# Performance work log

Hardware: AMD Instinct MI355X
Metric: run time of the kernel (lower is better)

The kernel has to match this reference:

```python
import jax, jax.numpy as jnp
import numpy as np

NUM_EMBEDDINGS = 4096
EMBEDDING_DIM = 512
N_TOKENS = 32768
COMMITMENT_COST = 0.25


def setup_inputs() -> dict:
    key = jax.random.key(0)
    k1, k2 = jax.random.split(key)
    flat_input = jax.random.normal(k1, (N_TOKENS, EMBEDDING_DIM), dtype=jnp.float32)
    # torch init: uniform(-1/K, 1/K)
    weight = jax.random.uniform(k2, (NUM_EMBEDDINGS, EMBEDDING_DIM), dtype=jnp.float32,
                                minval=-1.0 / NUM_EMBEDDINGS, maxval=1.0 / NUM_EMBEDDINGS)
    return {"flat_input": flat_input, "weight": weight}


def reference(flat_input, weight):
    distances = (jnp.sum(flat_input ** 2, axis=1, keepdims=True)
                 + jnp.sum(weight ** 2, axis=1)
                 - 2.0 * jnp.matmul(flat_input, weight.T))
    encoding_indices = jnp.argmin(distances, axis=1)  # [N]
    # one-hot @ weight == direct gather of codebook rows
    quantized = weight[encoding_indices]  # [N, D]

    e_latent_loss = jnp.mean((jax.lax.stop_gradient(quantized) - flat_input) ** 2, axis=1)
    q_latent_loss = jnp.mean((quantized - jax.lax.stop_gradient(flat_input)) ** 2, axis=1)
    loss = q_latent_loss + COMMITMENT_COST * e_latent_loss  # [N]

    # straight-through estimator
    quantized_st = flat_input + jax.lax.stop_gradient(quantized - flat_input)

    # avg_probs = mean of one-hot encodings over batch = normalized code counts
    counts = jnp.zeros((NUM_EMBEDDINGS,), dtype=flat_input.dtype).at[encoding_indices].add(1.0)
    avg_probs = counts / flat_input.shape[0]
    perplexity = jnp.exp(-jnp.sum(avg_probs * jnp.log(avg_probs + 1e-10)))

    return quantized_st, loss, perplexity, encoding_indices
```

## Files before the change

### kernel.cpp

```cpp
#include <hip/hip_runtime.h>
#include <math.h>

#define N_TOK 32768
#define K_CODES 4096
#define DIM 512
#define COMMIT 0.25f
#define NCAND 8
#define NSPLIT 2
#define SPLIT_CODES (K_CODES / NSPLIT)
#define NITER (SPLIT_CODES / 256)
#define BIAS 0.125f

typedef short s16x8 __attribute__((ext_vector_type(8)));
typedef float f32x4 __attribute__((ext_vector_type(4)));
typedef unsigned int uint32;
typedef unsigned long long u64;
typedef unsigned short u16;

__device__ __forceinline__ u16 f2bf(float f) {
    uint32 b = __float_as_uint(f);
    return (u16)((b + 0x7FFFu + ((b >> 16) & 1u)) >> 16);
}

__device__ __forceinline__ void gload16(const u16* g, u16* l) {
    __builtin_amdgcn_global_load_lds(
        (const __attribute__((address_space(1))) void*)g,
        (__attribute__((address_space(3))) void*)l,
        16, 0, 0);
}

__global__ __launch_bounds__(256) void tobf16_kernel(const float* __restrict__ src,
                                                     u16* __restrict__ dst, int n4) {
    int i = blockIdx.x * 256 + threadIdx.x;
    int stride = gridDim.x * 256;
    for (; i < n4; i += stride) {
        float4 v = ((const float4*)src)[i];
        ushort4 o;
        o.x = f2bf(v.x); o.y = f2bf(v.y); o.z = f2bf(v.z); o.w = f2bf(v.w);
        ((ushort4*)dst)[i] = o;
    }
}

__global__ __launch_bounds__(256) void rowsq_np_kernel(const float* __restrict__ a,
                                                       float* __restrict__ out,
                                                       int nrows) {
    #pragma clang fp contract(off)
    const int gw   = (blockIdx.x * 256 + threadIdx.x) >> 6;
    const int lane = threadIdx.x & 63;
    const int row  = gw * 8 + (lane >> 3);
    const int j    = lane & 7;
    if (row >= nrows) return;
    const float* p = a + (size_t)row * DIM;
    float blk[4];
    #pragma unroll
    for (int b = 0; b < 4; ++b) {
        const float* q = p + b * 128;
        float v = q[j];
        float r = v * v;
        for (int i = 8; i < 128; i += 8) { float u = q[i + j]; r += u * u; }
        float s1 = r  + __shfl_xor(r, 1);
        float s2 = s1 + __shfl_xor(s1, 2);
        float s3 = s2 + __shfl_xor(s2, 4);
        blk[b] = s3;
    }
    float res = (blk[0] + blk[1]) + (blk[2] + blk[3]);
    if (j == 0) out[row] = res;
}

__global__ __launch_bounds__(512, 1) void screen_kernel(const u16* __restrict__ xb,
                                                        const u16* __restrict__ wb,
                                                        const float* __restrict__ w2f,
                                                        u64* __restrict__ candPart) {
    __shared__ __attribute__((aligned(16))) u16 POOL[77824];

    const int tid  = threadIdx.x;
    const int wv   = tid >> 6;
    const int wt   = wv >> 2;
    const int wc   = wv & 3;
    const int lane = tid & 63;
    const int quad = lane >> 4;
    const int n15  = lane & 15;
    const int m0   = blockIdx.x * 128;
    const int sbase = blockIdx.y * SPLIT_CODES;

    const int l8  = lane >> 3;
    const int qsw = (lane & 7) ^ l8;

    const u16* xg0 = xb + (size_t)(m0 + wv * 16 + l8) * DIM + qsw * 8;
    const u16* xg1 = xg0 + (size_t)8 * DIM;
    const u16* wg0 = wb + (size_t)(sbase + wv * 32 + 0  + l8) * DIM + qsw * 8;
    const u16* wg1 = wg0 + (size_t)8 * DIM;
    const u16* wg2 = wg0 + (size_t)16 * DIM;
    const u16* wg3 = wg0 + (size_t)24 * DIM;

    {
        float* w2l = (float*)&POOL[73728];
        for (int i = tid; i < SPLIT_CODES; i += 512)
            w2l[i] = w2f[sbase + i] + BIAS;
    }

    uint32 r1[16], r2[16];
    #pragma unroll
    for (int i = 0; i < 16; ++i) { r1[i] = 0xFFFFFFFFu; r2[i] = 0xFFFFFFFFu; }

    f32x4 acc[4][4];
    #pragma unroll
    for (int i = 0; i < 4; ++i)
        #pragma unroll
        for (int c = 0; c < 4; ++c) acc[i][c] = (f32x4){0.f, 0.f, 0.f, 0.f};

    int xoff0[4], woff0[4], xoff1[4], woff1[4];
    #pragma unroll
    for (int i = 0; i < 4; ++i) {
        const int tr = wt * 64 + i * 16 + n15;
        xoff0[i] = tr * 64 + ((quad)     ^ (tr & 7)) * 8;
        xoff1[i] = tr * 64 + ((4 + quad) ^ (tr & 7)) * 8;
    }
    #pragma unroll
    for (int c = 0; c < 4; ++c) {
        const int cr = wc * 64 + c * 16 + n15;
        woff0[c] = cr * 64 + ((quad)     ^ (cr & 7)) * 8;
        woff1[c] = cr * 64 + ((4 + quad) ^ (cr & 7)) * 8;
    }

    #pragma unroll
    for (int tt = 0; tt < 2; ++tt) {
        const int ko = tt * 64;
        gload16(xg0 + ko, &POOL[tt * 8192 + wv * 1024]);
        gload16(xg1 + ko, &POOL[tt * 8192 + wv * 1024 + 512]);
        gload16(wg0 + ko, &POOL[24576 + tt * 16384 + wv * 2048]);
        gload16(wg1 + ko, &POOL[24576 + tt * 16384 + wv * 2048 + 512]);
        gload16(wg2 + ko, &POOL[24576 + tt * 16384 + wv * 2048 + 1024]);
        gload16(wg3 + ko, &POOL[24576 + tt * 16384 + wv * 2048 + 1536]);
    }
    __syncthreads();

    s16x8 pa[4], pb[4];
    #pragma unroll
    for (int i = 0; i < 4; ++i) pa[i] = *(const s16x8*)&POOL[xoff0[i]];
    #pragma unroll
    for (int c = 0; c < 4; ++c) pb[c] = *(const s16x8*)&POOL[24576 + woff0[c]];

    int bufc = 0;
    for (int t = 0; t < 64; ++t) {
        __syncthreads();

        if (t <= 61) {
            const int bn  = (bufc == 0) ? 2 : bufc - 1;
            const int tn  = t + 2;
            const size_t co = (size_t)(tn >> 3) * (256 * DIM) + (tn & 7) * 64;
            const size_t xo = (size_t)((tn & 7) * 64);
            gload16(xg0 + xo, &POOL[bn * 8192 + wv * 1024]);
            gload16(xg1 + xo, &POOL[bn * 8192 + wv * 1024 + 512]);
            gload16(wg0 + co, &POOL[24576 + bn * 16384 + wv * 2048]);
            gload16(wg1 + co, &POOL[24576 + bn * 16384 + wv * 2048 + 512]);
            gload16(wg2 + co, &POOL[24576 + bn * 16384 + wv * 2048 + 1024]);
            gload16(wg3 + co, &POOL[24576 + bn * 16384 + wv * 2048 + 1536]);
        }

        const u16* X = &POOL[bufc * 8192];
        const u16* W = &POOL[24576 + bufc * 16384];

        s16x8 qa[4], qb[4];
        #pragma unroll
        for (int i = 0; i < 4; ++i) qa[i] = *(const s16x8*)&X[xoff1[i]];
        #pragma unroll
        for (int c = 0; c < 4; ++c) qb[c] = *(const s16x8*)&W[woff1[c]];

        #pragma unroll
        for (int i = 0; i < 4; ++i)
            #pragma unroll
            for (int c = 0; c < 4; ++c)
                acc[i][c] = __builtin_amdgcn_mfma_f32_16x16x32_bf16(pa[i], pb[c], acc[i][c], 0, 0, 0);

        if (t < 63) {
            const int bn1 = (bufc == 2) ? 0 : bufc + 1;
            const u16* Xn = &POOL[bn1 * 8192];
            const u16* Wn = &POOL[24576 + bn1 * 16384];
            #pragma unroll
            for (int i = 0; i < 4; ++i) pa[i] = *(const s16x8*)&Xn[xoff0[i]];
            #pragma unroll
            for (int c = 0; c < 4; ++c) pb[c] = *(const s16x8*)&Wn[woff0[c]];
        }

        #pragma unroll
        for (int i = 0; i < 4; ++i)
            #pragma unroll
            for (int c = 0; c < 4; ++c)
                acc[i][c] = __builtin_amdgcn_mfma_f32_16x16x32_bf16(qa[i], qb[c], acc[i][c], 0, 0, 0);

        if ((t & 7) == 7) {
            const int it = t >> 3;
            const float* w2l = (const float*)&POOL[73728];
            float w2pb[4];
            #pragma unroll
            for (int c = 0; c < 4; ++c)
                w2pb[c] = w2l[it * 256 + wc * 64 + c * 16 + n15];
            #pragma unroll
            for (int i = 0; i < 4; ++i)
                #pragma unroll
                for (int r = 0; r < 4; ++r) {
                    const int ti = i * 4 + r;
                    #pragma unroll
                    for (int c = 0; c < 4; ++c) {
                        float s = fmaf(-2.0f, acc[i][c][r], w2pb[c]);
                        uint32 key = (__float_as_uint(s) & 0xFFFFFFC0u) | (uint32)((it << 2) | c);
                        uint32 mx = r1[ti] > key ? r1[ti] : key;
                        r1[ti] = r1[ti] < key ? r1[ti] : key;
                        r2[ti] = r2[ti] < mx ? r2[ti] : mx;
                    }
                }
            #pragma unroll
            for (int i = 0; i < 4; ++i)
                #pragma unroll
                for (int c = 0; c < 4; ++c) acc[i][c] = (f32x4){0.f, 0.f, 0.f, 0.f};
        }

        bufc = (bufc == 2) ? 0 : bufc + 1;
    }

    u64* MS = (u64*)POOL;
    for (int phase = 0; phase < 2; ++phase) {
        __syncthreads();
        if (wt == phase) {
            #pragma unroll
            for (int ti = 0; ti < 16; ++ti) {
                const int i = ti >> 2, r = ti & 3;
                const int tloc = i * 16 + quad * 4 + r;
                #pragma unroll
                for (int e = 0; e < 2; ++e) {
                    uint32 k  = e ? r2[ti] : r1[ti];
                    uint32 vb = k & 0xFFFFFFC0u;
                    uint32 id = k & 63u;
                    uint32 code = (uint32)(sbase + (id >> 2) * 256 + wc * 64 + (id & 3) * 16 + n15);
                    MS[tloc * 128 + (wc * 16 + n15) * 2 + e] = ((u64)vb << 32) | code;
                }
            }
        }
        __syncthreads();
        if (tid < 64) {
            u64 best[6];
            #pragma unroll
            for (int c = 0; c < 6; ++c) best[c] = 0xFFFFFFFFFFFFFFFFull;
            for (int e = 0; e < 128; ++e) {
                u64 v = MS[tid * 128 + e];
                if (v < best[5]) {
                    best[5] = v;
                    #pragma unroll
                    for (int p = 5; p > 0; --p)
                        if (best[p] < best[p - 1]) { u64 tv = best[p]; best[p] = best[p - 1]; best[p - 1] = tv; }
                }
            }
            const int token = m0 + phase * 64 + tid;
            u64* dst = candPart + ((size_t)blockIdx.y * N_TOK + token) * 6;
            #pragma unroll
            for (int c = 0; c < 6; ++c) dst[c] = best[c];
        }
    }
}

__global__ __launch_bounds__(256) void mergecand_kernel(const u64* __restrict__ candPart,
                                                        int* __restrict__ candF) {
    int t = blockIdx.x * 256 + threadIdx.x;
    u64 best[NCAND];
    #pragma unroll
    for (int c = 0; c < NCAND; ++c) best[c] = 0xFFFFFFFFFFFFFFFFull;
    for (int s = 0; s < NSPLIT; ++s) {
        const u64* src = candPart + ((size_t)s * N_TOK + t) * 6;
        #pragma unroll
        for (int c = 0; c < 6; ++c) {
            u64 v = src[c];
            if (v < best[NCAND - 1]) {
                best[NCAND - 1] = v;
                #pragma unroll
                for (int p = NCAND - 1; p > 0; --p)
                    if (best[p] < best[p - 1]) { u64 tv = best[p]; best[p] = best[p - 1]; best[p - 1] = tv; }
            }
        }
    }
    #pragma unroll
    for (int c = 0; c < NCAND; ++c) candF[(size_t)t * NCAND + c] = (int)(best[c] & 0xFFFu);
}

__global__ __launch_bounds__(256) void refine_kernel(const float* __restrict__ x,
                                                     const float* __restrict__ w,
                                                     const float* __restrict__ x2np,
                                                     const float* __restrict__ w2np,
                                                     const int* __restrict__ cand,
                                                     int* __restrict__ idx) {
    const int t    = blockIdx.x * 4 + (threadIdx.x >> 6);
    const int lane = threadIdx.x & 63;

    const float* xr = x + (size_t)t * DIM;
    float xv[8];
    #pragma unroll
    for (int j = 0; j < 8; ++j) xv[j] = xr[lane + 64 * j];
    const float x2 = x2np[t];

    float bd = 3.4e38f;
    int   bk = 0x7fffffff;
    for (int c = 0; c < NCAND; ++c) {
        int k = cand[(size_t)t * NCAND + c];
        const float* wr = w + (size_t)k * DIM;
        double m = 0.0;
        #pragma unroll
        for (int j = 0; j < 8; ++j)
            m = fma((double)xv[j], (double)wr[lane + 64 * j], m);
        #pragma unroll
        for (int off = 32; off >= 1; off >>= 1) m += __shfl_down(m, off);
        if (lane == 0) {
            #pragma clang fp contract(off)
            float m32 = (float)m;
            float T1  = x2 + w2np[k];
            float d   = T1 - 2.0f * m32;
            if (d < bd || (d == bd && k < bk)) { bd = d; bk = k; }
        }
    }
    if (lane == 0) idx[t] = bk;
}

__global__ __launch_bounds__(256) void gather_kernel(const float* __restrict__ x,
                                                     const float* __restrict__ w,
                                                     const int* __restrict__ idx,
                                                     float* __restrict__ out_q,
                                                     float* __restrict__ out_loss,
                                                     float* __restrict__ out_ind,
                                                     int* __restrict__ counts) {
    const int wave = threadIdx.x >> 6;
    const int lane = threadIdx.x & 63;
    const int token = blockIdx.x * 4 + wave;
    const int k = idx[token];

    const float4* xr = (const float4*)(x + (size_t)token * DIM);
    const float4* wr = (const float4*)(w + (size_t)k * DIM);
    float4*       qo = (float4*)(out_q + (size_t)token * DIM);

    float ss = 0.f;
    #pragma unroll
    for (int j = 0; j < 2; ++j) {
        int e = lane + j * 64;
        float4 xv = xr[e];
        float4 wv = wr[e];
        float4 d, o;
        d.x = wv.x - xv.x; o.x = xv.x + d.x;
        d.y = wv.y - xv.y; o.y = xv.y + d.y;
        d.z = wv.z - xv.z; o.z = xv.z + d.z;
        d.w = wv.w - xv.w; o.w = xv.w + d.w;
        ss += d.x * d.x + d.y * d.y + d.z * d.z + d.w * d.w;
        qo[e] = o;
    }
    #pragma unroll
    for (int off = 32; off >= 1; off >>= 1) ss += __shfl_down(ss, off);
    if (lane == 0) {
        float lm = ss * (1.0f / DIM);
        out_loss[token] = lm + COMMIT * lm;
        out_ind[token] = (float)k;
        atomicAdd(&counts[k], 1);
    }
}

__global__ __launch_bounds__(256) void perplex_kernel(const int* __restrict__ counts,
                                                      float* __restrict__ out2) {
    __shared__ double red[4];
    const int tid = threadIdx.x;
    const int lane = tid & 63;
    const int wid = tid >> 6;
    double s = 0.0;
    for (int t = tid; t < K_CODES; t += 256) {
        int c = counts[t];
        if (c) {
            double p = (double)c * (1.0 / N_TOK);
            s += p * log(p + 1e-10);
        }
    }
    #pragma unroll
    for (int off = 32; off >= 1; off >>= 1) s += __shfl_down(s, off);
    if (lane == 0) red[wid] = s;
    __syncthreads();
    if (tid == 0) {
        double t = red[0] + red[1] + red[2] + red[3];
        out2[0] = (float)exp(-t);
    }
}

extern "C" void kernel_launch(void* const* d_in, const int* in_sizes, int n_in,
                              void* d_out, int out_size, void* d_ws, size_t ws_size,
                              hipStream_t stream) {
    const float* x = (const float*)d_in[0];
    const float* w = (const float*)d_in[1];

    float* out0 = (float*)d_out;
    float* out1 = out0 + (size_t)N_TOK * DIM;
    float* out2 = out1 + N_TOK;
    float* out3 = out2 + 1;

    u64*   candPart = (u64*)d_ws;
    float* x2np     = (float*)(candPart + (size_t)NSPLIT * N_TOK * 6);
    float* w2np     = x2np + N_TOK;
    int*   idx      = (int*)(w2np + K_CODES);
    int*   counts   = idx + N_TOK;
    int*   candF    = counts + K_CODES;
    u16*   x_bf     = (u16*)(candF + (size_t)N_TOK * NCAND);
    u16*   w_bf     = x_bf + (size_t)N_TOK * DIM;

    hipMemsetAsync(counts, 0, K_CODES * sizeof(int), stream);

    tobf16_kernel<<<4096, 256, 0, stream>>>(x, x_bf, N_TOK * DIM / 4);
    tobf16_kernel<<<2048, 256, 0, stream>>>(w, w_bf, K_CODES * DIM / 4);
    rowsq_np_kernel<<<N_TOK / 32, 256, 0, stream>>>(x, x2np, N_TOK);
    rowsq_np_kernel<<<K_CODES / 32, 256, 0, stream>>>(w, w2np, K_CODES);
    screen_kernel<<<dim3(N_TOK / 128, NSPLIT), 512, 0, stream>>>(x_bf, w_bf, w2np, candPart);
    mergecand_kernel<<<N_TOK / 256, 256, 0, stream>>>(candPart, candF);
    refine_kernel<<<N_TOK / 4, 256, 0, stream>>>(x, w, x2np, w2np, candF, idx);
    gather_kernel<<<N_TOK / 4, 256, 0, stream>>>(x, w, idx, out0, out1, out3, counts);
    perplex_kernel<<<1, 256, 0, stream>>>(counts, out2);
}
```

Baseline: 439.3 us.

## Fuse prep conversions and merge/refine/gather into fewer kernels

Combines the bf16 conversion and row-norm passes into one prep kernel per matrix, so each input is read once per block instead of in two separate kernels. Merges the candidate merge, exact refine and gather/loss kernels into a single per-token kernel that keeps candidates in registers and reuses the chosen index via a shuffle. This removes four launches and the intermediate candF/idx round trips through global memory. In exchange, every lane of the fused kernel now performs the candidate merge redundantly.

Result: faster. 425.0 us (-3.3%).

```diff
diff --git a/kernel.cpp b/kernel.cpp
--- a/kernel.cpp
+++ b/kernel.cpp
@@ -29,28 +29,31 @@
         16, 0, 0);
 }
 
-__global__ __launch_bounds__(256) void tobf16_kernel(const float* __restrict__ src,
-                                                     u16* __restrict__ dst, int n4) {
-    int i = blockIdx.x * 256 + threadIdx.x;
-    int stride = gridDim.x * 256;
-    for (; i < n4; i += stride) {
-        float4 v = ((const float4*)src)[i];
-        ushort4 o;
-        o.x = f2bf(v.x); o.y = f2bf(v.y); o.z = f2bf(v.z); o.w = f2bf(v.w);
-        ((ushort4*)dst)[i] = o;
-    }
-}
-
-__global__ __launch_bounds__(256) void rowsq_np_kernel(const float* __restrict__ a,
-                                                       float* __restrict__ out,
-                                                       int nrows) {
+__global__ __launch_bounds__(256) void prep_kernel(const float* __restrict__ src,
+                                                   u16* __restrict__ bf,
+                                                   float* __restrict__ sq) {
     #pragma clang fp contract(off)
-    const int gw   = (blockIdx.x * 256 + threadIdx.x) >> 6;
-    const int lane = threadIdx.x & 63;
-    const int row  = gw * 8 + (lane >> 3);
+    const int tid  = threadIdx.x;
+    const int row0 = blockIdx.x * 32;
+
+    {
+        const float4* s4 = (const float4*)src + (size_t)row0 * 128;
+        ushort4*      d4 = (ushort4*)bf + (size_t)row0 * 128;
+        #pragma unroll
+        for (int i = 0; i < 16; ++i) {
+            int e = tid + i * 256;
+            float4 v = s4[e];
+            ushort4 o;
+            o.x = f2bf(v.x); o.y = f2bf(v.y); o.z = f2bf(v.z); o.w = f2bf(v.w);
+            d4[e] = o;
+        }
+    }
+
+    const int lane = tid & 63;
+    const int wvi  = tid >> 6;
+    const int row  = row0 + wvi * 8 + (lane >> 3);
     const int j    = lane & 7;
-    if (row >= nrows) return;
-    const float* p = a + (size_t)row * DIM;
+    const float* p = src + (size_t)row * DIM;
     float blk[4];
     #pragma unroll
     for (int b = 0; b < 4; ++b) {
@@ -64,7 +67,7 @@
         blk[b] = s3;
     }
     float res = (blk[0] + blk[1]) + (blk[2] + blk[3]);
-    if (j == 0) out[row] = res;
+    if (j == 0) sq[row] = res;
 }
 
 __global__ __launch_bounds__(512, 1) void screen_kernel(const u16* __restrict__ xb,
@@ -259,12 +262,19 @@
     }
 }
 
-__global__ __launch_bounds__(256) void mergecand_kernel(const u64* __restrict__ candPart,
-                                                        int* __restrict__ candF) {
-    int t = blockIdx.x * 256 + threadIdx.x;
+__global__ __launch_bounds__(256) void refine_gather_kernel(
+        const float* __restrict__ x, const float* __restrict__ w,
+        const float* __restrict__ x2np, const float* __restrict__ w2np,
+        const u64* __restrict__ candPart,
+        float* __restrict__ out_q, float* __restrict__ out_loss,
+        float* __restrict__ out_ind, int* __restrict__ counts) {
+    const int t    = blockIdx.x * 4 + (threadIdx.x >> 6);
+    const int lane = threadIdx.x & 63;
+
     u64 best[NCAND];
     #pragma unroll
     for (int c = 0; c < NCAND; ++c) best[c] = 0xFFFFFFFFFFFFFFFFull;
+    #pragma unroll
     for (int s = 0; s < NSPLIT; ++s) {
         const u64* src = candPart + ((size_t)s * N_TOK + t) * 6;
         #pragma unroll
@@ -278,18 +288,6 @@
             }
         }
     }
-    #pragma unroll
-    for (int c = 0; c < NCAND; ++c) candF[(size_t)t * NCAND + c] = (int)(best[c] & 0xFFFu);
-}
-
-__global__ __launch_bounds__(256) void refine_kernel(const float* __restrict__ x,
-                                                     const float* __restrict__ w,
-                                                     const float* __restrict__ x2np,
-                                                     const float* __restrict__ w2np,
-                                                     const int* __restrict__ cand,
-                                                     int* __restrict__ idx) {
-    const int t    = blockIdx.x * 4 + (threadIdx.x >> 6);
-    const int lane = threadIdx.x & 63;
 
     const float* xr = x + (size_t)t * DIM;
     float xv[8];
@@ -300,7 +298,7 @@
     float bd = 3.4e38f;
     int   bk = 0x7fffffff;
     for (int c = 0; c < NCAND; ++c) {
-        int k = cand[(size_t)t * NCAND + c];
+        int k = (int)(best[c] & 0xFFFu);
         const float* wr = w + (size_t)k * DIM;
         double m = 0.0;
         #pragma unroll
@@ -316,36 +314,23 @@
             if (d < bd || (d == bd && k < bk)) { bd = d; bk = k; }
         }
     }
-    if (lane == 0) idx[t] = bk;
-}
-
-__global__ __launch_bounds__(256) void gather_kernel(const float* __restrict__ x,
-                                                     const float* __restrict__ w,
-                                                     const int* __restrict__ idx,
-                                                     float* __restrict__ out_q,
-                                                     float* __restrict__ out_loss,
-                                                     float* __restrict__ out_ind,
-                                                     int* __restrict__ counts) {
-    const int wave = threadIdx.x >> 6;
-    const int lane = threadIdx.x & 63;
-    const int token = blockIdx.x * 4 + wave;
-    const int k = idx[token];
-
-    const float4* xr = (const float4*)(x + (size_t)token * DIM);
-    const float4* wr = (const float4*)(w + (size_t)k * DIM);
-    float4*       qo = (float4*)(out_q + (size_t)token * DIM);
+    const int kk = __shfl(bk, 0);
+
+    const float4* xr4 = (const float4*)(x + (size_t)t * DIM);
+    const float4* wr4 = (const float4*)(w + (size_t)kk * DIM);
+    float4*       qo  = (float4*)(out_q + (size_t)t * DIM);
 
     float ss = 0.f;
     #pragma unroll
     for (int j = 0; j < 2; ++j) {
         int e = lane + j * 64;
-        float4 xv = xr[e];
-        float4 wv = wr[e];
+        float4 xv4 = xr4[e];
+        float4 wv4 = wr4[e];
         float4 d, o;
-        d.x = wv.x - xv.x; o.x = xv.x + d.x;
-        d.y = wv.y - xv.y; o.y = xv.y + d.y;
-        d.z = wv.z - xv.z; o.z = xv.z + d.z;
-        d.w = wv.w - xv.w; o.w = xv.w + d.w;
+        d.x = wv4.x - xv4.x; o.x = xv4.x + d.x;
+        d.y = wv4.y - xv4.y; o.y = xv4.y + d.y;
+        d.z = wv4.z - xv4.z; o.z = xv4.z + d.z;
+        d.w = wv4.w - xv4.w; o.w = xv4.w + d.w;
         ss += d.x * d.x + d.y * d.y + d.z * d.z + d.w * d.w;
         qo[e] = o;
     }
@@ -353,9 +338,9 @@
     for (int off = 32; off >= 1; off >>= 1) ss += __shfl_down(ss, off);
     if (lane == 0) {
         float lm = ss * (1.0f / DIM);
-        out_loss[token] = lm + COMMIT * lm;
-        out_ind[token] = (float)k;
-        atomicAdd(&counts[k], 1);
+        out_loss[t] = lm + COMMIT * lm;
+        out_ind[t] = (float)kk;
+        atomicAdd(&counts[kk], 1);
     }
 }
 
@@ -405,13 +390,10 @@
 
     hipMemsetAsync(counts, 0, K_CODES * sizeof(int), stream);
 
-    tobf16_kernel<<<4096, 256, 0, stream>>>(x, x_bf, N_TOK * DIM / 4);
-    tobf16_kernel<<<2048, 256, 0, stream>>>(w, w_bf, K_CODES * DIM / 4);
-    rowsq_np_kernel<<<N_TOK / 32, 256, 0, stream>>>(x, x2np, N_TOK);
-    rowsq_np_kernel<<<K_CODES / 32, 256, 0, stream>>>(w, w2np, K_CODES);
+    prep_kernel<<<N_TOK / 32, 256, 0, stream>>>(x, x_bf, x2np);
+    prep_kernel<<<K_CODES / 32, 256, 0, stream>>>(w, w_bf, w2np);
     screen_kernel<<<dim3(N_TOK / 128, NSPLIT), 512, 0, stream>>>(x_bf, w_bf, w2np, candPart);
-    mergecand_kernel<<<N_TOK / 256, 256, 0, stream>>>(candPart, candF);
-    refine_kernel<<<N_TOK / 4, 256, 0, stream>>>(x, w, x2np, w2np, candF, idx);
-    gather_kernel<<<N_TOK / 4, 256, 0, stream>>>(x, w, idx, out0, out1, out3, counts);
+    refine_gather_kernel<<<N_TOK / 4, 256, 0, stream>>>(x, w, x2np, w2np, candPart,
+                                                        out0, out1, out3, counts);
     perplex_kernel<<<1, 256, 0, stream>>>(counts, out2);
 }
```
